# Kernel optimization log

Hardware: AMD Instinct MI355X
Metric: run time of the kernel (lower is better)

## Reference

```python
import jax, jax.numpy as jnp
import numpy as np

B, S, D, HD = 16, 2048, 1024, 64  # batch, seq, n_embd, head_dim


def setup_inputs() -> dict:
    key = jax.random.key(0)
    ks = jax.random.split(key, 4)
    std = 1.0 / np.sqrt(D)
    return {
        "x": jax.random.normal(ks[0], (B, S, D), dtype=jnp.float32),
        "Wq": jax.random.normal(ks[1], (D, HD), dtype=jnp.float32) * std,
        "bq": jnp.zeros((HD,), dtype=jnp.float32),
        "Wk": jax.random.normal(ks[2], (D, HD), dtype=jnp.float32) * std,
        "bk": jnp.zeros((HD,), dtype=jnp.float32),
        "Wv": jax.random.normal(ks[3], (D, HD), dtype=jnp.float32) * std,
        "bv": jnp.zeros((HD,), dtype=jnp.float32),
    }


def reference(x, Wq, bq, Wk, bk, Wv, bv):
    q = x @ Wq + bq  # [B,S,HD]
    k = x @ Wk + bk
    v = x @ Wv + bv
    scale = jnp.asarray(HD, x.dtype) ** -0.5
    scores = jnp.einsum("bqd,bkd->bqk", q, k) * scale  # [B,S,S]
    seq = x.shape[1]
    causal = jnp.tril(jnp.ones((seq, seq), dtype=bool))  # True = keep
    scores = jnp.where(causal, scores, jnp.asarray(-jnp.inf, scores.dtype))
    probs = jax.nn.softmax(scores, axis=-1)
    return jnp.einsum("bqk,bkd->bqd", probs, v)  # [B,S,HD]
```

## Files before the change

kernel.cpp:

```cpp
#include <hip/hip_runtime.h>
#include <hip/hip_bf16.h>
#include <math.h>

constexpr int Bsz  = 16;
constexpr int Seq  = 2048;
constexpr int Din  = 1024;
constexpr int Hd   = 64;
constexpr int Rows = Bsz * Seq;

typedef short  short8 __attribute__((ext_vector_type(8)));
typedef float  f32x4  __attribute__((ext_vector_type(4)));

__device__ __forceinline__ short bf16_bits(float f) {
    __hip_bfloat16 h = __float2bfloat16(f);
    return __builtin_bit_cast(short, h);
}

typedef __attribute__((address_space(1))) const void gvoid_t;
typedef __attribute__((address_space(3))) void lvoid_t;
__device__ __forceinline__ void gll16(const void* g, void* l) {
    __builtin_amdgcn_global_load_lds((gvoid_t*)g, (lvoid_t*)l, 16, 0, 0);
}

__global__ __launch_bounds__(256) void wt_prep(
    const float* __restrict__ Wq, const float* __restrict__ Wk,
    const float* __restrict__ Wv, short* __restrict__ Wf)
{
    const int u     = blockIdx.x * 256 + threadIdx.x;
    const int chunk = u / 768;
    const int rem   = u - chunk * 768;
    const int f     = rem >> 6;
    const int lane  = rem & 63;
    const int wg    = f >> 2, nt = f & 3;
    const int quad  = lane >> 4, l16 = lane & 15;
    const float* W  = (wg == 0) ? Wq : (wg == 1) ? Wk : Wv;
    const int k0 = chunk * 32 + quad * 8;
    const int n  = nt * 16 + l16;
    short8 v;
    #pragma unroll
    for (int j = 0; j < 8; ++j) v[j] = bf16_bits(W[(size_t)(k0 + j) * Hd + n]);
    *(short8*)(Wf + (size_t)u * 8) = v;
}

__global__ __launch_bounds__(256) void qkv_kernel(
    const float* __restrict__ x,
    const short* __restrict__ Wf,
    const float* __restrict__ bq, const float* __restrict__ bk,
    const float* __restrict__ bv,
    short* __restrict__ Qf, short* __restrict__ Kf, short* __restrict__ Vf)
{
    const int tid  = threadIdx.x;
    const int wave = tid >> 6;
    const int lane = tid & 63;
    const int quad = lane >> 4;
    const int l16  = lane & 15;
    const int bx   = blockIdx.x;
    const int m0   = bx * 64;

    __shared__ __align__(16) short smem[14336];
    short* sW = smem;

    const float* xrow = x + (size_t)(m0 + wave * 16 + l16) * Din + quad * 8;

    f32x4 acc[12] = {};

    {
        const short* g = Wf + wave * 1536 + lane * 8;
        short*       l = sW + wave * 1536;
        gll16(g,        l);
        gll16(g +  512, l +  512);
        gll16(g + 1024, l + 1024);
    }
    float4 a0 = *(const float4*)(xrow);
    float4 a1 = *(const float4*)(xrow + 4);
    __syncthreads();

    for (int c = 0; c < 32; ++c) {
        const int cur = (c & 1) * 6144;
        if (c < 31) {
            const short* g = Wf + (size_t)(c + 1) * 6144 + wave * 1536 + lane * 8;
            short*       l = sW + (cur ^ 6144) + wave * 1536;
            gll16(g,        l);
            gll16(g +  512, l +  512);
            gll16(g + 1024, l + 1024);
        }
        float4 b0 = a0, b1 = a1;
        if (c < 31) {
            b0 = *(const float4*)(xrow + (c + 1) * 32);
            b1 = *(const float4*)(xrow + (c + 1) * 32 + 4);
        }
        short8 af;
        af[0] = bf16_bits(a0.x); af[1] = bf16_bits(a0.y);
        af[2] = bf16_bits(a0.z); af[3] = bf16_bits(a0.w);
        af[4] = bf16_bits(a1.x); af[5] = bf16_bits(a1.y);
        af[6] = bf16_bits(a1.z); af[7] = bf16_bits(a1.w);
        const short* wsrc = sW + cur + lane * 8;
        #pragma unroll
        for (int f = 0; f < 12; ++f) {
            const short8 bb = *(const short8*)(wsrc + f * 512);
            acc[f] = __builtin_amdgcn_mfma_f32_16x16x32_bf16(af, bb, acc[f], 0, 0, 0);
        }
        a0 = b0; a1 = b1;
        __syncthreads();
    }

    short (*eS)[2][16 * 72] = reinterpret_cast<short(*)[2][16 * 72]>(smem);
    short* eV = smem + 9216;

    #pragma unroll
    for (int wg = 0; wg < 2; ++wg) {
        const float* bias = wg ? bk : bq;
        #pragma unroll
        for (int nt = 0; nt < 4; ++nt) {
            const float bb = bias[nt * 16 + l16];
            #pragma unroll
            for (int r = 0; r < 4; ++r)
                eS[wave][wg][(quad * 4 + r) * 72 + nt * 16 + l16] =
                    bf16_bits(acc[wg * 4 + nt][r] + bb);
        }
    }
    #pragma unroll
    for (int wg = 0; wg < 2; ++wg) {
        const short8 v0 = *(const short8*)&eS[wave][wg][l16 * 72 + quad * 8];
        const short8 v1 = *(const short8*)&eS[wave][wg][l16 * 72 + 32 + quad * 8];
        if (wg == 0) {
            const size_t tg = (size_t)bx * 4 + wave;
            *(short8*)(Qf + (tg * 2 + 0) * 512 + lane * 8) = v0;
            *(short8*)(Qf + (tg * 2 + 1) * 512 + lane * 8) = v1;
        } else {
            *(short8*)(Kf + (((size_t)bx * 2 + 0) * 4 + wave) * 512 + lane * 8) = v0;
            *(short8*)(Kf + (((size_t)bx * 2 + 1) * 4 + wave) * 512 + lane * 8) = v1;
        }
    }

    #pragma unroll
    for (int nt = 0; nt < 4; ++nt) {
        const float bb = bv[nt * 16 + l16];
        #pragma unroll
        for (int r = 0; r < 4; ++r)
            eV[(nt * 16 + l16) * 80 + wave * 16 + quad * 4 + r] =
                bf16_bits(acc[8 + nt][r] + bb);
    }
    __syncthreads();
    #pragma unroll
    for (int s = 0; s < 2; ++s) {
        const int slot   = tid + s * 256;
        const int lane_s = slot & 63;
        const int u      = slot >> 6;
        const int th     = u >> 2, ntd = u & 3;
        const int q_s    = lane_s >> 4, l_s = lane_s & 15;
        const short8 v = *(const short8*)&eV[(ntd * 16 + l_s) * 80 + th * 32 + q_s * 8];
        *(short8*)(Vf + (((size_t)bx * 2 + th) * 4 + ntd) * 512 + lane_s * 8) = v;
    }
}

__global__ __launch_bounds__(256) void attn_kernel(
    const short* __restrict__ Qf, const short* __restrict__ Kf,
    const short* __restrict__ Vf, float* __restrict__ out)
{
    const int tid  = threadIdx.x;
    const int wave = tid >> 6;
    const int lane = tid & 63;
    const int quad = lane >> 4;
    const int l16  = lane & 15;
    const int b    = blockIdx.y;
    const int bx   = blockIdx.x;
    const int qs   = (bx & 1) ? (127 - (bx >> 1)) : (bx >> 1);
    const int dTile = qs >> 2;
    const int tiles = dTile + 1;
    const int qoff  = (qs & 3) * 16;

    __shared__ __align__(16) unsigned char sm[17408 + 512];
    short* Ps   = (short*)sm;
    float* Obuf = (float*)sm;
    float* mb   = (float*)(sm + 17408);
    float* lb   = mb + 64;

    const size_t tg = (size_t)b * 128 + qs;
    const short8 qf0 = *(const short8*)(Qf + (tg * 2 + 0) * 512 + lane * 8);
    const short8 qf1 = *(const short8*)(Qf + (tg * 2 + 1) * 512 + lane * 8);

    f32x4 o[4] = {};
    float m_run[4], l_run[4];
    #pragma unroll
    for (int r = 0; r < 4; ++r) { m_run[r] = -INFINITY; l_run[r] = 0.0f; }

    const float C = 0.125f * 1.44269504088896340736f;

    for (int kt = wave; kt < tiles; kt += 4) {
        const short* ktile = Kf + (size_t)(b * 32 + kt) * 4096;
        const short* vtile = Vf + (size_t)(b * 32 + kt) * 4096;

        f32x4 s[4] = {};
        __builtin_amdgcn_s_setprio(1);
        #pragma unroll
        for (int nt = 0; nt < 4; ++nt) {
            const short8 kf0 = *(const short8*)(ktile + ((0 * 4 + nt) * 64 + lane) * 8);
            const short8 kf1 = *(const short8*)(ktile + ((1 * 4 + nt) * 64 + lane) * 8);
            s[nt] = __builtin_amdgcn_mfma_f32_16x16x32_bf16(qf0, kf0, s[nt], 0, 0, 0);
            s[nt] = __builtin_amdgcn_mfma_f32_16x16x32_bf16(qf1, kf1, s[nt], 0, 0, 0);
        }
        __builtin_amdgcn_s_setprio(0);

        if (kt == dTile) {
            #pragma unroll
            for (int nt = 0; nt < 4; ++nt) {
                const int kg = nt * 16 + l16;
                #pragma unroll
                for (int r = 0; r < 4; ++r) {
                    const int qg = qoff + quad * 4 + r;
                    s[nt][r] = (kg <= qg) ? s[nt][r] * C : -INFINITY;
                }
            }
        } else {
            #pragma unroll
            for (int nt = 0; nt < 4; ++nt)
                #pragma unroll
                for (int r = 0; r < 4; ++r) s[nt][r] *= C;
        }

        float rm[4];
        #pragma unroll
        for (int r = 0; r < 4; ++r)
            rm[r] = fmaxf(fmaxf(s[0][r], s[1][r]), fmaxf(s[2][r], s[3][r]));
        #pragma unroll
        for (int off = 1; off < 16; off <<= 1)
            #pragma unroll
            for (int r = 0; r < 4; ++r)
                rm[r] = fmaxf(rm[r], __shfl_xor(rm[r], off));

        float alpha[4];
        #pragma unroll
        for (int r = 0; r < 4; ++r) {
            const float mn = fmaxf(m_run[r], rm[r]);
            alpha[r] = exp2f(m_run[r] - mn);
            m_run[r] = mn;
        }

        float rs[4] = {0.f, 0.f, 0.f, 0.f};
        #pragma unroll
        for (int nt = 0; nt < 4; ++nt)
            #pragma unroll
            for (int r = 0; r < 4; ++r) {
                const float p = exp2f(s[nt][r] - m_run[r]);
                s[nt][r] = p;
                rs[r] += p;
            }
        #pragma unroll
        for (int off = 1; off < 16; off <<= 1)
            #pragma unroll
            for (int r = 0; r < 4; ++r)
                rs[r] += __shfl_xor(rs[r], off);
        #pragma unroll
        for (int r = 0; r < 4; ++r) l_run[r] = l_run[r] * alpha[r] + rs[r];

        #pragma unroll
        for (int r = 0; r < 4; ++r) {
            o[0][r] *= alpha[r]; o[1][r] *= alpha[r];
            o[2][r] *= alpha[r]; o[3][r] *= alpha[r];
        }

        #pragma unroll
        for (int nt = 0; nt < 4; ++nt)
            #pragma unroll
            for (int r = 0; r < 4; ++r)
                Ps[wave * 1152 + (quad * 4 + r) * 72 + nt * 16 + l16] = bf16_bits(s[nt][r]);

        const short8 pf0 = *(const short8*)&Ps[wave * 1152 + l16 * 72 + quad * 8];
        const short8 pf1 = *(const short8*)&Ps[wave * 1152 + l16 * 72 + 32 + quad * 8];

        __builtin_amdgcn_s_setprio(1);
        #pragma unroll
        for (int nt = 0; nt < 4; ++nt) {
            const short8 vA = *(const short8*)(vtile + ((0 * 4 + nt) * 64 + lane) * 8);
            const short8 vB = *(const short8*)(vtile + ((1 * 4 + nt) * 64 + lane) * 8);
            o[nt] = __builtin_amdgcn_mfma_f32_16x16x32_bf16(pf0, vA, o[nt], 0, 0, 0);
            o[nt] = __builtin_amdgcn_mfma_f32_16x16x32_bf16(pf1, vB, o[nt], 0, 0, 0);
        }
        __builtin_amdgcn_s_setprio(0);
    }

    if (l16 == 0) {
        #pragma unroll
        for (int r = 0; r < 4; ++r) mb[wave * 16 + quad * 4 + r] = m_run[r];
    }
    __syncthreads();

    float fac[4];
    #pragma unroll
    for (int r = 0; r < 4; ++r) {
        const int row = quad * 4 + r;
        const float mg = fmaxf(fmaxf(mb[row], mb[16 + row]),
                               fmaxf(mb[32 + row], mb[48 + row]));
        fac[r] = exp2f(m_run[r] - mg);
    }
    if (l16 == 0) {
        #pragma unroll
        for (int r = 0; r < 4; ++r) lb[wave * 16 + quad * 4 + r] = l_run[r] * fac[r];
    }
    #pragma unroll
    for (int nt = 0; nt < 4; ++nt)
        #pragma unroll
        for (int r = 0; r < 4; ++r)
            Obuf[wave * 1088 + (quad * 4 + r) * 68 + nt * 16 + l16] = o[nt][r] * fac[r];
    __syncthreads();

    {
        const int row = tid >> 4;
        const int c0  = (tid & 15) * 4;
        const float lsum = lb[row] + lb[16 + row] + lb[32 + row] + lb[48 + row];
        float4 a = *(const float4*)&Obuf[0 * 1088 + row * 68 + c0];
        const float4 a1 = *(const float4*)&Obuf[1 * 1088 + row * 68 + c0];
        const float4 a2 = *(const float4*)&Obuf[2 * 1088 + row * 68 + c0];
        const float4 a3 = *(const float4*)&Obuf[3 * 1088 + row * 68 + c0];
        a.x += a1.x + a2.x + a3.x;  a.y += a1.y + a2.y + a3.y;
        a.z += a1.z + a2.z + a3.z;  a.w += a1.w + a2.w + a3.w;
        const float inv = 1.0f / lsum;
        float4 r4 = make_float4(a.x * inv, a.y * inv, a.z * inv, a.w * inv);
        *(float4*)(out + ((size_t)b * Seq + qs * 16 + row) * Hd + c0) = r4;
    }
}

extern "C" void kernel_launch(void* const* d_in, const int* in_sizes, int n_in,
                              void* d_out, int out_size, void* d_ws, size_t ws_size,
                              hipStream_t stream)
{
    const float* x  = (const float*)d_in[0];
    const float* Wq = (const float*)d_in[1];
    const float* bq = (const float*)d_in[2];
    const float* Wk = (const float*)d_in[3];
    const float* bk = (const float*)d_in[4];
    const float* Wv = (const float*)d_in[5];
    const float* bv = (const float*)d_in[6];
    float* out = (float*)d_out;

    short* Qf = (short*)d_ws;
    short* Kf = Qf + (size_t)Rows * Hd;
    short* Vf = Kf + (size_t)Rows * Hd;
    short* Wf = Vf + (size_t)Rows * Hd;

    wt_prep<<<96, 256, 0, stream>>>(Wq, Wk, Wv, Wf);
    qkv_kernel<<<512, 256, 0, stream>>>(x, Wf, bq, bk, bv, Qf, Kf, Vf);
    attn_kernel<<<dim3(128, 16), 256, 0, stream>>>(Qf, Kf, Vf, out);
}
```

Measured before the change: 275.4 us.

## Halve QKV block rows and split output columns across wave pairs

The QKV projection kernel now processes 32 rows per block instead of 64, with pairs of waves sharing the same 16 x-rows and each wave computing half of the 192 output columns. The grid doubles to 1024 blocks and per-wave accumulators drop from 12 to 6, which is meant to improve occupancy and load balance across CUs. In exchange, each x row is loaded by two waves, so global reads of x double per block. The W tile is also reloaded per block, so total weight traffic doubles. The epilogue is reworked so K and V fragments are scattered in the tile layout the attention kernel expects.

```diff
diff --git a/kernel.cpp b/kernel.cpp
--- a/kernel.cpp
+++ b/kernel.cpp
@@ -54,22 +54,24 @@
     const int lane = tid & 63;
     const int quad = lane >> 4;
     const int l16  = lane & 15;
+    const int g    = wave >> 1;
+    const int h    = wave & 1;
     const int bx   = blockIdx.x;
-    const int m0   = bx * 64;
-
-    __shared__ __align__(16) short smem[14336];
+    const int m0   = bx * 32;
+
+    __shared__ __align__(16) short smem[12288];
     short* sW = smem;
 
-    const float* xrow = x + (size_t)(m0 + wave * 16 + l16) * Din + quad * 8;
-
-    f32x4 acc[12] = {};
+    const float* xrow = x + (size_t)(m0 + g * 16 + l16) * Din + quad * 8;
+
+    f32x4 acc[6] = {};
 
     {
-        const short* g = Wf + wave * 1536 + lane * 8;
-        short*       l = sW + wave * 1536;
-        gll16(g,        l);
-        gll16(g +  512, l +  512);
-        gll16(g + 1024, l + 1024);
+        const short* gp = Wf + wave * 1536 + lane * 8;
+        short*       lp = sW + wave * 1536;
+        gll16(gp,        lp);
+        gll16(gp +  512, lp +  512);
+        gll16(gp + 1024, lp + 1024);
     }
     float4 a0 = *(const float4*)(xrow);
     float4 a1 = *(const float4*)(xrow + 4);
@@ -78,11 +80,11 @@
     for (int c = 0; c < 32; ++c) {
         const int cur = (c & 1) * 6144;
         if (c < 31) {
-            const short* g = Wf + (size_t)(c + 1) * 6144 + wave * 1536 + lane * 8;
-            short*       l = sW + (cur ^ 6144) + wave * 1536;
-            gll16(g,        l);
-            gll16(g +  512, l +  512);
-            gll16(g + 1024, l + 1024);
+            const short* gp = Wf + (size_t)(c + 1) * 6144 + wave * 1536 + lane * 8;
+            short*       lp = sW + (cur ^ 6144) + wave * 1536;
+            gll16(gp,        lp);
+            gll16(gp +  512, lp +  512);
+            gll16(gp + 1024, lp + 1024);
         }
         float4 b0 = a0, b1 = a1;
         if (c < 31) {
@@ -94,63 +96,74 @@
         af[2] = bf16_bits(a0.z); af[3] = bf16_bits(a0.w);
         af[4] = bf16_bits(a1.x); af[5] = bf16_bits(a1.y);
         af[6] = bf16_bits(a1.z); af[7] = bf16_bits(a1.w);
-        const short* wsrc = sW + cur + lane * 8;
-        #pragma unroll
-        for (int f = 0; f < 12; ++f) {
-            const short8 bb = *(const short8*)(wsrc + f * 512);
-            acc[f] = __builtin_amdgcn_mfma_f32_16x16x32_bf16(af, bb, acc[f], 0, 0, 0);
+        const short* wsrc = sW + cur + h * 3072 + lane * 8;
+        #pragma unroll
+        for (int i = 0; i < 6; ++i) {
+            const short8 bb = *(const short8*)(wsrc + i * 512);
+            acc[i] = __builtin_amdgcn_mfma_f32_16x16x32_bf16(af, bb, acc[i], 0, 0, 0);
         }
         a0 = b0; a1 = b1;
         __syncthreads();
     }
 
-    short (*eS)[2][16 * 72] = reinterpret_cast<short(*)[2][16 * 72]>(smem);
-    short* eV = smem + 9216;
-
-    #pragma unroll
-    for (int wg = 0; wg < 2; ++wg) {
-        const float* bias = wg ? bk : bq;
+    short (*eS)[2][1152] = reinterpret_cast<short(*)[2][1152]>(smem);
+    short* eV = smem + 4608;
+
+    if (h == 0) {
         #pragma unroll
         for (int nt = 0; nt < 4; ++nt) {
-            const float bb = bias[nt * 16 + l16];
-            #pragma unroll
-            for (int r = 0; r < 4; ++r)
-                eS[wave][wg][(quad * 4 + r) * 72 + nt * 16 + l16] =
-                    bf16_bits(acc[wg * 4 + nt][r] + bb);
-        }
-    }
-    #pragma unroll
-    for (int wg = 0; wg < 2; ++wg) {
-        const short8 v0 = *(const short8*)&eS[wave][wg][l16 * 72 + quad * 8];
-        const short8 v1 = *(const short8*)&eS[wave][wg][l16 * 72 + 32 + quad * 8];
-        if (wg == 0) {
-            const size_t tg = (size_t)bx * 4 + wave;
-            *(short8*)(Qf + (tg * 2 + 0) * 512 + lane * 8) = v0;
-            *(short8*)(Qf + (tg * 2 + 1) * 512 + lane * 8) = v1;
-        } else {
-            *(short8*)(Kf + (((size_t)bx * 2 + 0) * 4 + wave) * 512 + lane * 8) = v0;
-            *(short8*)(Kf + (((size_t)bx * 2 + 1) * 4 + wave) * 512 + lane * 8) = v1;
-        }
-    }
-
-    #pragma unroll
-    for (int nt = 0; nt < 4; ++nt) {
-        const float bb = bv[nt * 16 + l16];
-        #pragma unroll
-        for (int r = 0; r < 4; ++r)
-            eV[(nt * 16 + l16) * 80 + wave * 16 + quad * 4 + r] =
-                bf16_bits(acc[8 + nt][r] + bb);
+            const float bb = bq[nt * 16 + l16];
+            #pragma unroll
+            for (int r = 0; r < 4; ++r)
+                eS[g][0][(quad * 4 + r) * 72 + nt * 16 + l16] =
+                    bf16_bits(acc[nt][r] + bb);
+        }
+        #pragma unroll
+        for (int nt = 0; nt < 2; ++nt) {
+            const float bb = bk[nt * 16 + l16];
+            #pragma unroll
+            for (int r = 0; r < 4; ++r)
+                eS[g][1][(quad * 4 + r) * 72 + nt * 16 + l16] =
+                    bf16_bits(acc[4 + nt][r] + bb);
+        }
+        const short8 v0 = *(const short8*)&eS[g][0][l16 * 72 + quad * 8];
+        const short8 v1 = *(const short8*)&eS[g][0][l16 * 72 + 32 + quad * 8];
+        const size_t tg = (size_t)bx * 2 + g;
+        *(short8*)(Qf + (tg * 2 + 0) * 512 + lane * 8) = v0;
+        *(short8*)(Qf + (tg * 2 + 1) * 512 + lane * 8) = v1;
+    } else {
+        #pragma unroll
+        for (int nt = 0; nt < 2; ++nt) {
+            const float bb = bk[(2 + nt) * 16 + l16];
+            #pragma unroll
+            for (int r = 0; r < 4; ++r)
+                eS[g][1][(quad * 4 + r) * 72 + (2 + nt) * 16 + l16] =
+                    bf16_bits(acc[nt][r] + bb);
+        }
+        #pragma unroll
+        for (int nt = 0; nt < 4; ++nt) {
+            const float bb = bv[nt * 16 + l16];
+            #pragma unroll
+            for (int r = 0; r < 4; ++r)
+                eV[(nt * 16 + l16) * 44 + g * 16 + quad * 4 + r] =
+                    bf16_bits(acc[2 + nt][r] + bb);
+        }
     }
     __syncthreads();
-    #pragma unroll
-    for (int s = 0; s < 2; ++s) {
-        const int slot   = tid + s * 256;
-        const int lane_s = slot & 63;
-        const int u      = slot >> 6;
-        const int th     = u >> 2, ntd = u & 3;
-        const int q_s    = lane_s >> 4, l_s = lane_s & 15;
-        const short8 v = *(const short8*)&eV[(ntd * 16 + l_s) * 80 + th * 32 + q_s * 8];
-        *(short8*)(Vf + (((size_t)bx * 2 + th) * 4 + ntd) * 512 + lane_s * 8) = v;
+
+    if (h == 0) {
+        const short8 v0 = *(const short8*)&eS[g][1][l16 * 72 + quad * 8];
+        const short8 v1 = *(const short8*)&eS[g][1][l16 * 72 + 32 + quad * 8];
+        const size_t t  = bx >> 1;
+        const int    nt = (bx & 1) * 2 + g;
+        *(short8*)(Kf + ((t * 2 + 0) * 4 + nt) * 512 + lane * 8) = v0;
+        *(short8*)(Kf + ((t * 2 + 1) * 4 + nt) * 512 + lane * 8) = v1;
+    }
+    {
+        const size_t t  = bx >> 1;
+        const int    ks = bx & 1;
+        const short8 v  = *(const short8*)&eV[(wave * 16 + l16) * 44 + quad * 8];
+        *(short8*)(Vf + ((t * 2 + ks) * 4 + wave) * 512 + lane * 8) = v;
     }
 }
 
@@ -340,6 +353,6 @@
     short* Wf = Vf + (size_t)Rows * Hd;
 
     wt_prep<<<96, 256, 0, stream>>>(Wq, Wk, Wv, Wf);
-    qkv_kernel<<<512, 256, 0, stream>>>(x, Wf, bq, bk, bv, Qf, Kf, Vf);
+    qkv_kernel<<<1024, 256, 0, stream>>>(x, Wf, bq, bk, bv, Qf, Kf, Vf);
     attn_kernel<<<dim3(128, 16), 256, 0, stream>>>(Qf, Kf, Vf, out);
 }
```

New measurement: 288.9 us. 4.9% more time.
